# Performance work log

Measured on AMD Instinct MI355X. Metric: run time of the kernel, lower is better.

The kernel has to match this reference:

```python
import jax, jax.numpy as jnp
import numpy as np

WEIGHT = 1.0
_EPS = 0.008856          # (6/29)^3 threshold used by skimage rgb2lab
_KAPPA = 7.787           # 1/3 * (29/6)^2 scaled form used by skimage
# sRGB -> XYZ (D65) luminance (Y) row of the conversion matrix, as in skimage
_YR, _YG, _YB = 0.2126729, 0.7151522, 0.0721750


def _luminance_L(rgb):
    """rgb: (B,3,H,W) in [-1,1] -> L channel of CIE Lab, shape (B,H,W)."""
    s = (rgb + 1.0) * 0.5                                   # to [0,1]
    # inverse sRGB companding (gamma expansion)
    lin = jnp.where(s > 0.04045, ((s + 0.055) / 1.055) ** 2.4, s / 12.92)
    Y = _YR * lin[:, 0] + _YG * lin[:, 1] + _YB * lin[:, 2]  # (B,H,W), Yn=1
    # f(Y): cube root above threshold, linear segment below (safe-where for grads)
    Y_safe = jnp.where(Y > _EPS, Y, 1.0)
    f = jnp.where(Y > _EPS, jnp.cbrt(Y_safe), _KAPPA * Y + 16.0 / 116.0)
    return 116.0 * f - 16.0                                  # L in [0,100]


def setup_inputs() -> dict:
    key = jax.random.key(0)
    k1, k2 = jax.random.split(key)
    shape = (64, 3, 512, 512)
    generated = jax.random.uniform(k1, shape, dtype=jnp.float32, minval=-1.0, maxval=1.0)
    target = jax.random.uniform(k2, shape, dtype=jnp.float32, minval=-1.0, maxval=1.0)
    return {"generated": generated, "target": target}


def reference(generated, target):
    L_gen = _luminance_L(generated)
    L_tgt = _luminance_L(target)
    loss = jnp.mean(jnp.abs(L_gen - L_tgt))  # F.l1_loss
    return WEIGHT * loss
```

## Files before the change

### kernel.cpp

```cpp
#include <hip/hip_runtime.h>


#define HW4   65536
#define CHW4  196608
#define NPIX  16777216

__device__ __forceinline__ float fast_log2(float x) {
#if __has_builtin(__builtin_amdgcn_logf)
    return __builtin_amdgcn_logf(x);
#else
    return __log2f(x);
#endif
}
__device__ __forceinline__ float fast_exp2(float x) {
#if __has_builtin(__builtin_amdgcn_exp2f)
    return __builtin_amdgcn_exp2f(x);
#else
    return exp2f(x);
#endif
}

__device__ __forceinline__ float srgb_expand(float x) {
    float a  = fmaf(x, 0.47393364f, 0.52606636f);
    float hi = fast_exp2(2.4f * fast_log2(a));
    float lo = fmaf(x, 0.03869969f, 0.03869969f);
    return (x > -0.9191f) ? hi : lo;
}

__device__ __forceinline__ float lab_f(float r, float g, float b) {
    float lr = srgb_expand(r);
    float lg = srgb_expand(g);
    float lb = srgb_expand(b);
    float Y  = fmaf(0.2126729f, lr, fmaf(0.7151522f, lg, 0.0721750f * lb));
    float cb = fast_exp2(0.333333333333f * fast_log2(Y));
    float lin = fmaf(7.787f, Y, 16.0f / 116.0f);
    return (Y > 0.008856f) ? cb : lin;
}

__device__ __forceinline__ float group_absdiff(
        float4 gr, float4 gg, float4 gb,
        float4 tr, float4 tg, float4 tb) {
    float s;
    s  = fabsf(lab_f(gr.x, gg.x, gb.x) - lab_f(tr.x, tg.x, tb.x));
    s += fabsf(lab_f(gr.y, gg.y, gb.y) - lab_f(tr.y, tg.y, tb.y));
    s += fabsf(lab_f(gr.z, gg.z, gb.z) - lab_f(tr.z, tg.z, tb.z));
    s += fabsf(lab_f(gr.w, gg.w, gb.w) - lab_f(tr.w, tg.w, tb.w));
    return s;
}

__global__ void zero_out_kernel(float* out) {
    if (threadIdx.x == 0) out[0] = 0.0f;
}

__global__ __launch_bounds__(512, 4) void lum_loss_kernel(
        const float* __restrict__ gen,
        const float* __restrict__ tgt,
        float* __restrict__ out) {
    const float4* gp = (const float4*)gen;
    const float4* tp = (const float4*)tgt;

    int t    = blockIdx.x * 512 + threadIdx.x;
    int g0   = t << 1;
    int b    = g0 >> 16;
    int i    = g0 & 65535;
    int base = b * CHW4 + i;

    float4 gr0 = gp[base];
    float4 gr1 = gp[base + 1];
    float4 gg0 = gp[base + HW4];
    float4 gg1 = gp[base + HW4 + 1];
    float4 gb0 = gp[base + 2 * HW4];
    float4 gb1 = gp[base + 2 * HW4 + 1];
    float4 tr0 = tp[base];
    float4 tr1 = tp[base + 1];
    float4 tg0 = tp[base + HW4];
    float4 tg1 = tp[base + HW4 + 1];
    float4 tb0 = tp[base + 2 * HW4];
    float4 tb1 = tp[base + 2 * HW4 + 1];

    float a = group_absdiff(gr0, gg0, gb0, tr0, tg0, tb0)
            + group_absdiff(gr1, gg1, gb1, tr1, tg1, tb1);
    a *= 116.0f;

    #pragma unroll
    for (int off = 32; off > 0; off >>= 1)
        a += __shfl_down(a, off, 64);

    __shared__ float smem[8];
    int lane = threadIdx.x & 63;
    int wave = threadIdx.x >> 6;
    if (lane == 0) smem[wave] = a;
    __syncthreads();

    if (threadIdx.x == 0) {
        float s = ((smem[0] + smem[1]) + (smem[2] + smem[3]))
                + ((smem[4] + smem[5]) + (smem[6] + smem[7]));
        atomicAdd(out, s * (1.0f / (float)NPIX));
    }
}

extern "C" void kernel_launch(void* const* d_in, const int* in_sizes, int n_in,
                              void* d_out, int out_size, void* d_ws, size_t ws_size,
                              hipStream_t stream) {
    const float* gen = (const float*)d_in[0];
    const float* tgt = (const float*)d_in[1];
    float* out = (float*)d_out;

    zero_out_kernel<<<1, 64, 0, stream>>>(out);
    lum_loss_kernel<<<4096, 512, 0, stream>>>(gen, tgt, out);
}
```

Before: 387.4 us.

## Split per-thread work into two halves with inline-asm loads and staged waitcnt

Each thread now processes one float4 group from the first half of the pixel space and one from the second half, so adjacent lanes read adjacent float4s and coalescing improves. Loads are issued with inline global_load_dwordx4 asm, and explicit s_waitcnt vmcnt(6)/vmcnt(0) with sched barriers let computation on the first half overlap the second half's outstanding loads. The launch_bounds occupancy hint is relaxed. The risk is that inline asm hides the loads from the compiler, and the manual waitcnt may not match what the compiler itself emits.

Result: no change. 388.3 us (+0.2%).

```diff
diff --git a/kernel.cpp b/kernel.cpp
--- a/kernel.cpp
+++ b/kernel.cpp
@@ -3,6 +3,7 @@
 
 #define HW4   65536
 #define CHW4  196608
+#define HALFG 2097152
 #define NPIX  16777216
 
 __device__ __forceinline__ float fast_log2(float x) {
@@ -48,38 +49,49 @@
     return s;
 }
 
+__device__ __forceinline__ float4 gload(const float4* p) {
+    float4 r;
+    asm volatile("global_load_dwordx4 %0, %1, off" : "=v"(r) : "v"(p));
+    return r;
+}
+
 __global__ void zero_out_kernel(float* out) {
     if (threadIdx.x == 0) out[0] = 0.0f;
 }
 
-__global__ __launch_bounds__(512, 4) void lum_loss_kernel(
+__global__ __launch_bounds__(512) void lum_loss_kernel(
         const float* __restrict__ gen,
         const float* __restrict__ tgt,
         float* __restrict__ out) {
     const float4* gp = (const float4*)gen;
     const float4* tp = (const float4*)tgt;
 
-    int t    = blockIdx.x * 512 + threadIdx.x;
-    int g0   = t << 1;
-    int b    = g0 >> 16;
-    int i    = g0 & 65535;
-    int base = b * CHW4 + i;
+    int t  = blockIdx.x * 512 + threadIdx.x;
+    int ga = t;
+    int gb = t + HALFG;
+    int basea = (ga >> 16) * CHW4 + (ga & 65535);
+    int baseb = (gb >> 16) * CHW4 + (gb & 65535);
 
-    float4 gr0 = gp[base];
-    float4 gr1 = gp[base + 1];
-    float4 gg0 = gp[base + HW4];
-    float4 gg1 = gp[base + HW4 + 1];
-    float4 gb0 = gp[base + 2 * HW4];
-    float4 gb1 = gp[base + 2 * HW4 + 1];
-    float4 tr0 = tp[base];
-    float4 tr1 = tp[base + 1];
-    float4 tg0 = tp[base + HW4];
-    float4 tg1 = tp[base + HW4 + 1];
-    float4 tb0 = tp[base + 2 * HW4];
-    float4 tb1 = tp[base + 2 * HW4 + 1];
+    float4 agr = gload(gp + basea);
+    float4 agg = gload(gp + basea + HW4);
+    float4 agb = gload(gp + basea + 2 * HW4);
+    float4 atr = gload(tp + basea);
+    float4 atg = gload(tp + basea + HW4);
+    float4 atb = gload(tp + basea + 2 * HW4);
+    float4 bgr = gload(gp + baseb);
+    float4 bgg = gload(gp + baseb + HW4);
+    float4 bgb = gload(gp + baseb + 2 * HW4);
+    float4 btr = gload(tp + baseb);
+    float4 btg = gload(tp + baseb + HW4);
+    float4 btb = gload(tp + baseb + 2 * HW4);
 
-    float a = group_absdiff(gr0, gg0, gb0, tr0, tg0, tb0)
-            + group_absdiff(gr1, gg1, gb1, tr1, tg1, tb1);
+    asm volatile("s_waitcnt vmcnt(6)" ::: "memory");
+    __builtin_amdgcn_sched_barrier(0);
+    float a = group_absdiff(agr, agg, agb, atr, atg, atb);
+
+    asm volatile("s_waitcnt vmcnt(0)" ::: "memory");
+    __builtin_amdgcn_sched_barrier(0);
+    a += group_absdiff(bgr, bgg, bgb, btr, btg, btb);
     a *= 116.0f;
 
     #pragma unroll
```
